# Optimization experiments

Hardware: AMD Instinct MI355X
Metric: run time of the kernel (lower is better)

Reference implementation:

```python
import jax, jax.numpy as jnp
import numpy as np

HARD_RATIO = 0.5
HARD_WEIGHT = 0.5
B, Q, D = 1024, 32, 512


def _l2norm(x):
    return x / jnp.linalg.norm(x, axis=-1, keepdims=True)


def setup_inputs() -> dict:
    key = jax.random.key(0)
    k1, k2 = jax.random.split(key)
    fusion_feats = _l2norm(jax.random.normal(k1, (B, D), dtype=jnp.float32))
    target_feats = _l2norm(jax.random.normal(k2, (B, Q, D), dtype=jnp.float32))
    temp = jnp.float32(0.07)
    return {"fusion_feats": fusion_feats, "target_feats": target_feats, "temp": temp}


def reference(fusion_feats, target_feats, temp):
    b = fusion_feats.shape[0]
    # sim[i, j, q] = fusion[i] . target[j, q]  -> max over query tokens q
    sim = jnp.einsum('id,jqd->ijq', fusion_feats, target_feats)  # (B, B, Q)
    sim_max = jnp.max(sim, axis=-1) / temp                        # (B, B)

    # standard InfoNCE with diagonal labels
    loss_standard = -jnp.mean(jnp.diagonal(jax.nn.log_softmax(sim_max, axis=-1)))

    # online hard-negative mining: per-row top-k over off-diagonal entries
    num_hard = max(1, int(b * HARD_RATIO))
    diag_mask = jnp.eye(b, dtype=bool)
    masked = jnp.where(diag_mask, -jnp.inf, sim_max)
    hard_sims, _ = jax.lax.top_k(masked, num_hard)                # (B, num_hard)
    pos = jnp.diagonal(sim_max)                                    # (B,)
    # -log(exp(pos) / (exp(pos) + sum exp(hard))) = logsumexp([pos, hard]) - pos
    lse = jax.nn.logsumexp(jnp.concatenate([pos[:, None], hard_sims], axis=1), axis=1)
    hard_loss_online = jnp.mean(lse - pos)

    total_loss = loss_standard + HARD_WEIGHT * hard_loss_online
    return total_loss
```

## Files before the change

kernel.cpp:

```cpp
#include <hip/hip_runtime.h>
#include <hip/hip_bf16.h>
#include <math.h>

typedef unsigned short u16;
typedef unsigned int u32;
typedef __attribute__((ext_vector_type(4))) float f32x4;
typedef __attribute__((ext_vector_type(8))) __bf16 bf16x8;

__device__ __forceinline__ u16 f2bf(float x) {
    unsigned u = __float_as_uint(x);
    u += 0x7fffu + ((u >> 16) & 1u);
    return (u16)(u >> 16);
}
__device__ __forceinline__ unsigned pk(float lo, float hi) {
    return (unsigned)f2bf(lo) | ((unsigned)f2bf(hi) << 16);
}

__global__ void cvt_fused(const float* __restrict__ F, const float* __restrict__ T,
                          u16* __restrict__ Fb, u16* __restrict__ Tb,
                          float* __restrict__ out) {
    const int idx = blockIdx.x * blockDim.x + threadIdx.x;
    if (idx == 0) out[0] = 0.f;
    const float* s;
    u16* d;
    int i;
    if (idx < 65536) { s = F; d = Fb; i = idx * 8; }
    else             { s = T; d = Tb; i = (idx - 65536) * 8; }
    float4 v0 = *(const float4*)(s + i);
    float4 v1 = *(const float4*)(s + i + 4);
    uint4 o;
    o.x = pk(v0.x, v0.y); o.y = pk(v0.z, v0.w);
    o.z = pk(v1.x, v1.y); o.w = pk(v1.z, v1.w);
    *(uint4*)(d + i) = o;
}

#define GLB_AS __attribute__((address_space(1)))
#define LDS_AS __attribute__((address_space(3)))

__device__ __forceinline__ void gload_lds16(const void* g, void* l) {
    __builtin_amdgcn_global_load_lds((const GLB_AS void*)g, (LDS_AS void*)l, 16, 0, 0);
}

__global__ __launch_bounds__(256, 2)
void gemm_max(const u16* __restrict__ A, const u16* __restrict__ B,
              const float* __restrict__ temp_ptr, float* __restrict__ sim) {
    __shared__ __align__(16) u16 lA[128 * 64];
    __shared__ __align__(16) u16 lB[128 * 64];
    const int bn = blockIdx.x;
    const int bm = blockIdx.y;
    const int tid  = threadIdx.x;
    const int wave = tid >> 6;
    const int lane = tid & 63;
    const int wm = wave >> 1;
    const int wn = wave & 1;

    f32x4 acc[4][4] = {};

    const int srow = lane >> 3;
    const int skc  = ((lane & 7) ^ srow) << 3;
    const u16* gA0 = A + (size_t)(bm * 128 + wave * 8 + srow) * 512 + skc;
    const u16* gB0 = B + (size_t)(bn * 128 + wave * 8 + srow) * 512 + skc;
    u16* dA = lA + wave * 512;
    u16* dB = lB + wave * 512;

    const int frow  = lane & 15;
    const int fq    = lane >> 4;
    const int abase = ((frow >> 3) * 512) + ((frow & 7) * 64);
    const int c0    = (fq ^ (frow & 7)) << 3;

    for (int k0 = 0; k0 < 512; k0 += 64) {
#pragma unroll
        for (int j = 0; j < 4; ++j) {
            gload_lds16(gA0 + k0 + j * (32 * 512), dA + j * 2048);
            gload_lds16(gB0 + k0 + j * (32 * 512), dB + j * 2048);
        }
        __syncthreads();
#pragma unroll
        for (int h = 0; h < 2; ++h) {
            const int co = c0 ^ (h << 5);
            bf16x8 af[4], bf[4];
#pragma unroll
            for (int t = 0; t < 4; ++t) {
                af[t] = *(const bf16x8*)&lA[wm * 4096 + t * 1024 + abase + co];
                bf[t] = *(const bf16x8*)&lB[wn * 4096 + t * 1024 + abase + co];
            }
#pragma unroll
            for (int mt = 0; mt < 4; ++mt)
#pragma unroll
                for (int nt = 0; nt < 4; ++nt)
                    acc[mt][nt] = __builtin_amdgcn_mfma_f32_16x16x32_bf16(
                        af[mt], bf[nt], acc[mt][nt], 0, 0, 0);
        }
        __syncthreads();
    }

    const float tempv = *temp_ptr;
    const int jb = (bn * 128 + wn * 64) >> 5;
#pragma unroll
    for (int mt = 0; mt < 4; ++mt) {
#pragma unroll
        for (int rr = 0; rr < 4; ++rr) {
            float v0 = fmaxf(acc[mt][0][rr], acc[mt][1][rr]);
            float v1 = fmaxf(acc[mt][2][rr], acc[mt][3][rr]);
#pragma unroll
            for (int off = 1; off < 16; off <<= 1) {
                v0 = fmaxf(v0, __shfl_xor(v0, off));
                v1 = fmaxf(v1, __shfl_xor(v1, off));
            }
            if ((lane & 15) == 0) {
                const int row = bm * 128 + wm * 64 + mt * 16 + fq * 4 + rr;
                sim[row * 1024 + jb]     = v0 / tempv;
                sim[row * 1024 + jb + 1] = v1 / tempv;
            }
        }
    }
}

__device__ __forceinline__ u32 f2key(float x) {
    u32 b = __float_as_uint(x);
    return (b & 0x80000000u) ? ~b : (b | 0x80000000u);
}
__device__ __forceinline__ float key2f(u32 k) {
    return __uint_as_float((k & 0x80000000u) ? (k & 0x7fffffffu) : ~k);
}

__global__ __launch_bounds__(256)
void row_loss(const float* __restrict__ sim, float* __restrict__ out) {
    __shared__ u32 hist[4 * 256];
    const int tid = threadIdx.x;
    const int lane = tid & 63;
    const int wv = tid >> 6;
    const int i = blockIdx.x * 4 + wv;
    u32* h = hist + wv * 256;

    float v[16];
    const float4* rp = (const float4*)(sim + (size_t)i * 1024);
#pragma unroll
    for (int t = 0; t < 4; ++t) {
        float4 f = rp[t * 64 + lane];
        v[t * 4 + 0] = f.x; v[t * 4 + 1] = f.y; v[t * 4 + 2] = f.z; v[t * 4 + 3] = f.w;
    }

    const int dslot = ((i >> 8) << 2) | (i & 3);
    const int dlane = (i >> 2) & 63;

    u32 k[16];
#pragma unroll
    for (int t = 0; t < 16; ++t) {
        u32 kk = f2key(v[t]);
        k[t] = (lane == dlane && t == dslot) ? 0u : kk;
    }

    float pv = 0.f;
#pragma unroll
    for (int t = 0; t < 16; ++t) if (t == dslot) pv = v[t];
    const float pos = __shfl(pv, dlane);

    float m = v[0];
#pragma unroll
    for (int t = 1; t < 16; ++t) m = fmaxf(m, v[t]);
#pragma unroll
    for (int off = 32; off > 0; off >>= 1) m = fmaxf(m, __shfl_xor(m, off));
    float s = 0.f;
#pragma unroll
    for (int t = 0; t < 16; ++t) s += __expf(v[t] - m);
#pragma unroll
    for (int off = 32; off > 0; off >>= 1) s += __shfl_xor(s, off);

    const float loss_std = m + __logf(s) - pos;

    u32 prefix = 0;
    u32 r = 512;
#pragma unroll
    for (int d = 3; d >= 0; --d) {
        *(uint4*)(h + lane * 4) = uint4{0u, 0u, 0u, 0u};
        __builtin_amdgcn_wave_barrier();
#pragma unroll
        for (int t = 0; t < 16; ++t) {
            bool act = true;
            if (d < 3) act = ((k[t] >> (8 * (d + 1))) == prefix);
            if (act) atomicAdd(&h[(k[t] >> (8 * d)) & 255u], 1u);
        }
        __builtin_amdgcn_wave_barrier();
        uint4 c = *(const uint4*)(h + lane * 4);
        u32 local = c.x + c.y + c.z + c.w;
        u32 S = local;
#pragma unroll
        for (int off = 1; off < 64; off <<= 1) {
            u32 tmp = __shfl_down(S, off);
            if (lane + off < 64) S += tmp;
        }
        const u32 above = S - local;
        const u32 cg3 = above + c.w;
        const u32 cg2 = cg3 + c.z;
        const u32 cg1 = cg2 + c.y;
        const u32 cg0 = cg1 + c.x;
        int q = -1;
        if      (cg3 >= r) q = 3;
        else if (cg2 >= r) q = 2;
        else if (cg1 >= r) q = 1;
        else if (cg0 >= r) q = 0;
        int cand = (q >= 0) ? (lane * 4 + q) : -1;
#pragma unroll
        for (int off = 32; off > 0; off >>= 1) cand = max(cand, __shfl_xor(cand, off));
        const u32 cgq = (q == 3) ? cg3 : (q == 2) ? cg2 : (q == 1) ? cg1 : cg0;
        const u32 cq  = (q == 3) ? c.w : (q == 2) ? c.z : (q == 1) ? c.y : c.x;
        const u32 rp_local = r - (cgq - cq);
        r = __shfl(rp_local, cand >> 2);
        prefix = (prefix << 8) | (u32)cand;
    }

    const u32 t_key = prefix;
    const float tval = key2f(t_key);

    float se = 0.f;
    int cgt = 0;
#pragma unroll
    for (int t = 0; t < 16; ++t) {
        if (k[t] > t_key) { se += __expf(v[t] - m); ++cgt; }
    }
#pragma unroll
    for (int off = 32; off > 0; off >>= 1) se += __shfl_xor(se, off);
#pragma unroll
    for (int off = 32; off > 0; off >>= 1) cgt += __shfl_xor(cgt, off);

    const float sh = se + (float)(512 - cgt) * __expf(tval - m) + __expf(pos - m);
    const float hard = m + __logf(sh) - pos;

    if (lane == 0)
        atomicAdd(out, (loss_std + 0.5f * hard) * (1.0f / 1024.0f));
}

extern "C" void kernel_launch(void* const* d_in, const int* in_sizes, int n_in,
                              void* d_out, int out_size, void* d_ws, size_t ws_size,
                              hipStream_t stream) {
    const float* F    = (const float*)d_in[0];
    const float* T    = (const float*)d_in[1];
    const float* temp = (const float*)d_in[2];
    float* out = (float*)d_out;

    char* ws = (char*)d_ws;
    u16*  Fb  = (u16*)ws;
    u16*  Tb  = (u16*)(ws + (1u << 20));
    float* sim = (float*)(ws + (1u << 20) + (32u << 20));

    cvt_fused<<<8448, 256, 0, stream>>>(F, T, Fb, Tb, out);

    dim3 grid(256, 8);
    gemm_max<<<grid, 256, 0, stream>>>(Fb, Tb, temp, sim);

    row_loss<<<256, 256, 0, stream>>>(sim, out);
}
```

Baseline: 169.3 us.

## Switch similarity GEMM to FP8 scaled MFMA and use binary-search top-k threshold

Inputs are converted to FP8 (e4m3, pre-scaled by 16) instead of bf16. The GEMM then uses the 16x16x128 f8f6f4 scaled MFMA with a 128-deep K tile, which halves operand bytes and the number of K iterations. Results are rescaled by 1/(256*temp). The row-loss radix-select over LDS histograms is replaced by a 32-step bisection on the order-preserving keys, using wave-wide count reductions. FP8 lowers the accuracy of the similarity values, which may shift which entries fall in the top-k and risks tolerance failures. The bisection trades LDS atomics for more iterations.

After: 162.3 us. -4.1%, faster.

```diff
diff --git a/kernel.cpp b/kernel.cpp
--- a/kernel.cpp
+++ b/kernel.cpp
@@ -3,35 +3,29 @@
 #include <math.h>
 
 typedef unsigned short u16;
+typedef unsigned char u8;
 typedef unsigned int u32;
 typedef __attribute__((ext_vector_type(4))) float f32x4;
-typedef __attribute__((ext_vector_type(8))) __bf16 bf16x8;
-
-__device__ __forceinline__ u16 f2bf(float x) {
-    unsigned u = __float_as_uint(x);
-    u += 0x7fffu + ((u >> 16) & 1u);
-    return (u16)(u >> 16);
-}
-__device__ __forceinline__ unsigned pk(float lo, float hi) {
-    return (unsigned)f2bf(lo) | ((unsigned)f2bf(hi) << 16);
-}
+typedef __attribute__((ext_vector_type(8))) int i32x8;
 
 __global__ void cvt_fused(const float* __restrict__ F, const float* __restrict__ T,
-                          u16* __restrict__ Fb, u16* __restrict__ Tb,
+                          u32* __restrict__ Fb, u32* __restrict__ Tb,
                           float* __restrict__ out) {
     const int idx = blockIdx.x * blockDim.x + threadIdx.x;
     if (idx == 0) out[0] = 0.f;
     const float* s;
-    u16* d;
+    u32* d;
     int i;
-    if (idx < 65536) { s = F; d = Fb; i = idx * 8; }
-    else             { s = T; d = Tb; i = (idx - 65536) * 8; }
-    float4 v0 = *(const float4*)(s + i);
-    float4 v1 = *(const float4*)(s + i + 4);
-    uint4 o;
-    o.x = pk(v0.x, v0.y); o.y = pk(v0.z, v0.w);
-    o.z = pk(v1.x, v1.y); o.w = pk(v1.z, v1.w);
-    *(uint4*)(d + i) = o;
+    if (idx < 65536) { s = F; d = Fb; i = idx; }
+    else             { s = T; d = Tb; i = idx - 65536; }
+    const float4 v0 = *(const float4*)(s + (size_t)i * 8);
+    const float4 v1 = *(const float4*)(s + (size_t)i * 8 + 4);
+    int lo = __builtin_amdgcn_cvt_pk_fp8_f32(v0.x * 16.f, v0.y * 16.f, 0, false);
+    lo     = __builtin_amdgcn_cvt_pk_fp8_f32(v0.z * 16.f, v0.w * 16.f, lo, true);
+    int hi = __builtin_amdgcn_cvt_pk_fp8_f32(v1.x * 16.f, v1.y * 16.f, 0, false);
+    hi     = __builtin_amdgcn_cvt_pk_fp8_f32(v1.z * 16.f, v1.w * 16.f, hi, true);
+    uint2 o; o.x = (u32)lo; o.y = (u32)hi;
+    ((uint2*)d)[i] = o;
 }
 
 #define GLB_AS __attribute__((address_space(1)))
@@ -42,10 +36,10 @@
 }
 
 __global__ __launch_bounds__(256, 2)
-void gemm_max(const u16* __restrict__ A, const u16* __restrict__ B,
+void gemm_max(const u8* __restrict__ A, const u8* __restrict__ B,
               const float* __restrict__ temp_ptr, float* __restrict__ sim) {
-    __shared__ __align__(16) u16 lA[128 * 64];
-    __shared__ __align__(16) u16 lB[128 * 64];
+    __shared__ __align__(16) u8 lA[128 * 128];
+    __shared__ __align__(16) u8 lB[128 * 128];
     const int bn = blockIdx.x;
     const int bm = blockIdx.y;
     const int tid  = threadIdx.x;
@@ -57,44 +51,50 @@
     f32x4 acc[4][4] = {};
 
     const int srow = lane >> 3;
-    const int skc  = ((lane & 7) ^ srow) << 3;
-    const u16* gA0 = A + (size_t)(bm * 128 + wave * 8 + srow) * 512 + skc;
-    const u16* gB0 = B + (size_t)(bn * 128 + wave * 8 + srow) * 512 + skc;
-    u16* dA = lA + wave * 512;
-    u16* dB = lB + wave * 512;
-
-    const int frow  = lane & 15;
-    const int fq    = lane >> 4;
-    const int abase = ((frow >> 3) * 512) + ((frow & 7) * 64);
-    const int c0    = (fq ^ (frow & 7)) << 3;
-
-    for (int k0 = 0; k0 < 512; k0 += 64) {
+    const int sch  = (lane & 7) ^ srow;
+    const u8* gA0 = A + (size_t)(bm * 128 + wave * 8 + srow) * 512 + sch * 16;
+    const u8* gB0 = B + (size_t)(bn * 128 + wave * 8 + srow) * 512 + sch * 16;
+    u8* dA = lA + wave * 1024;
+    u8* dB = lB + wave * 1024;
+
+    const int frow = lane & 15;
+    const int fq   = lane >> 4;
+
+    union Frag { int4 h[2]; i32x8 v; };
+
+    for (int k0 = 0; k0 < 512; k0 += 128) {
 #pragma unroll
         for (int j = 0; j < 4; ++j) {
-            gload_lds16(gA0 + k0 + j * (32 * 512), dA + j * 2048);
-            gload_lds16(gB0 + k0 + j * (32 * 512), dB + j * 2048);
+            gload_lds16(gA0 + k0 + j * 16384, dA + j * 4096);
+            gload_lds16(gB0 + k0 + j * 16384, dB + j * 4096);
         }
         __syncthreads();
-#pragma unroll
-        for (int h = 0; h < 2; ++h) {
-            const int co = c0 ^ (h << 5);
-            bf16x8 af[4], bf[4];
-#pragma unroll
-            for (int t = 0; t < 4; ++t) {
-                af[t] = *(const bf16x8*)&lA[wm * 4096 + t * 1024 + abase + co];
-                bf[t] = *(const bf16x8*)&lB[wn * 4096 + t * 1024 + abase + co];
-            }
-#pragma unroll
-            for (int mt = 0; mt < 4; ++mt)
-#pragma unroll
-                for (int nt = 0; nt < 4; ++nt)
-                    acc[mt][nt] = __builtin_amdgcn_mfma_f32_16x16x32_bf16(
-                        af[mt], bf[nt], acc[mt][nt], 0, 0, 0);
+
+        Frag af[4], bf[4];
+#pragma unroll
+        for (int t = 0; t < 4; ++t) {
+            const int ra = wm * 64 + t * 16 + frow;
+            const int ba = ((ra >> 3) << 10) + ((ra & 7) << 7);
+            af[t].h[0] = *(const int4*)&lA[ba + ((((fq << 1))     ^ (ra & 7)) << 4)];
+            af[t].h[1] = *(const int4*)&lA[ba + ((((fq << 1) | 1) ^ (ra & 7)) << 4)];
+            const int rb = wn * 64 + t * 16 + frow;
+            const int bb = ((rb >> 3) << 10) + ((rb & 7) << 7);
+            bf[t].h[0] = *(const int4*)&lB[bb + ((((fq << 1))     ^ (rb & 7)) << 4)];
+            bf[t].h[1] = *(const int4*)&lB[bb + ((((fq << 1) | 1) ^ (rb & 7)) << 4)];
         }
+#pragma unroll
+        for (int mt = 0; mt < 4; ++mt)
+#pragma unroll
+            for (int nt = 0; nt < 4; ++nt)
+                acc[mt][nt] = __builtin_amdgcn_mfma_scale_f32_16x16x128_f8f6f4(
+                    af[mt].v, bf[nt].v, acc[mt][nt],
+                    0, 0,
+                    0, 0x7F,
+                    0, 0x7F);
         __syncthreads();
     }
 
-    const float tempv = *temp_ptr;
+    const float inv = 1.0f / (256.0f * (*temp_ptr));
     const int jb = (bn * 128 + wn * 64) >> 5;
 #pragma unroll
     for (int mt = 0; mt < 4; ++mt) {
@@ -109,8 +109,8 @@
             }
             if ((lane & 15) == 0) {
                 const int row = bm * 128 + wm * 64 + mt * 16 + fq * 4 + rr;
-                sim[row * 1024 + jb]     = v0 / tempv;
-                sim[row * 1024 + jb + 1] = v1 / tempv;
+                sim[row * 1024 + jb]     = v0 * inv;
+                sim[row * 1024 + jb + 1] = v1 * inv;
             }
         }
     }
@@ -126,12 +126,10 @@
 
 __global__ __launch_bounds__(256)
 void row_loss(const float* __restrict__ sim, float* __restrict__ out) {
-    __shared__ u32 hist[4 * 256];
     const int tid = threadIdx.x;
     const int lane = tid & 63;
     const int wv = tid >> 6;
     const int i = blockIdx.x * 4 + wv;
-    u32* h = hist + wv * 256;
 
     float v[16];
     const float4* rp = (const float4*)(sim + (size_t)i * 1024);
@@ -166,51 +164,20 @@
     for (int t = 0; t < 16; ++t) s += __expf(v[t] - m);
 #pragma unroll
     for (int off = 32; off > 0; off >>= 1) s += __shfl_xor(s, off);
-
     const float loss_std = m + __logf(s) - pos;
 
-    u32 prefix = 0;
-    u32 r = 512;
-#pragma unroll
-    for (int d = 3; d >= 0; --d) {
-        *(uint4*)(h + lane * 4) = uint4{0u, 0u, 0u, 0u};
-        __builtin_amdgcn_wave_barrier();
-#pragma unroll
-        for (int t = 0; t < 16; ++t) {
-            bool act = true;
-            if (d < 3) act = ((k[t] >> (8 * (d + 1))) == prefix);
-            if (act) atomicAdd(&h[(k[t] >> (8 * d)) & 255u], 1u);
-        }
-        __builtin_amdgcn_wave_barrier();
-        uint4 c = *(const uint4*)(h + lane * 4);
-        u32 local = c.x + c.y + c.z + c.w;
-        u32 S = local;
-#pragma unroll
-        for (int off = 1; off < 64; off <<= 1) {
-            u32 tmp = __shfl_down(S, off);
-            if (lane + off < 64) S += tmp;
-        }
-        const u32 above = S - local;
-        const u32 cg3 = above + c.w;
-        const u32 cg2 = cg3 + c.z;
-        const u32 cg1 = cg2 + c.y;
-        const u32 cg0 = cg1 + c.x;
-        int q = -1;
-        if      (cg3 >= r) q = 3;
-        else if (cg2 >= r) q = 2;
-        else if (cg1 >= r) q = 1;
-        else if (cg0 >= r) q = 0;
-        int cand = (q >= 0) ? (lane * 4 + q) : -1;
-#pragma unroll
-        for (int off = 32; off > 0; off >>= 1) cand = max(cand, __shfl_xor(cand, off));
-        const u32 cgq = (q == 3) ? cg3 : (q == 2) ? cg2 : (q == 1) ? cg1 : cg0;
-        const u32 cq  = (q == 3) ? c.w : (q == 2) ? c.z : (q == 1) ? c.y : c.x;
-        const u32 rp_local = r - (cgq - cq);
-        r = __shfl(rp_local, cand >> 2);
-        prefix = (prefix << 8) | (u32)cand;
-    }
-
-    const u32 t_key = prefix;
+    u32 lo = 0u, hi = 0xFFFFFFFFu;
+    while (lo < hi) {
+        const u32 span = hi - lo;
+        const u32 mid = lo + (span >> 1) + (span & 1u);
+        int cnt = 0;
+#pragma unroll
+        for (int t = 0; t < 16; ++t) cnt += (k[t] >= mid);
+#pragma unroll
+        for (int off = 32; off > 0; off >>= 1) cnt += __shfl_xor(cnt, off);
+        if (cnt >= 512) lo = mid; else hi = mid - 1;
+    }
+    const u32 t_key = lo;
     const float tval = key2f(t_key);
 
     float se = 0.f;
@@ -240,14 +207,14 @@
     float* out = (float*)d_out;
 
     char* ws = (char*)d_ws;
-    u16*  Fb  = (u16*)ws;
-    u16*  Tb  = (u16*)(ws + (1u << 20));
+    u32*  Fb8 = (u32*)ws;
+    u32*  Tb8 = (u32*)(ws + (1u << 20));
     float* sim = (float*)(ws + (1u << 20) + (32u << 20));
 
-    cvt_fused<<<8448, 256, 0, stream>>>(F, T, Fb, Tb, out);
+    cvt_fused<<<8448, 256, 0, stream>>>(F, T, Fb8, Tb8, out);
 
     dim3 grid(256, 8);
-    gemm_max<<<grid, 256, 0, stream>>>(Fb, Tb, temp, sim);
+    gemm_max<<<grid, 256, 0, stream>>>((const u8*)Fb8, (const u8*)Tb8, temp, sim);
 
     row_loss<<<256, 256, 0, stream>>>(sim, out);
 }
```
